# Performance work log

Measured on AMD Instinct MI355X. Metric: run time of the kernel, lower is better.

Reference implementation:

```python
import jax, jax.numpy as jnp
import numpy as np

NEG_INF = jnp.float32(-1e30)


def setup_inputs() -> dict:
    key = jax.random.key(0)
    ks = jax.random.split(key, 7)
    B, Lx, Lm, d = 4, 256, 256, 256
    return {
        "x": jax.random.normal(ks[0], (B, Lx, d), dtype=jnp.float32),
        "memory": jax.random.normal(ks[1], (B, Lm, d), dtype=jnp.float32),
        "memory_mask": jax.random.randint(ks[2], (B, Lm), 0, 2, dtype=jnp.int32),
        "ws1_w": jax.random.normal(ks[3], (d, d), dtype=jnp.float32) * 0.05,
        "ws1_b": jax.random.normal(ks[4], (d,), dtype=jnp.float32) * 0.05,
        "ws2_w": jax.random.normal(ks[5], (d, d), dtype=jnp.float32) * 0.05,
        "wst_w": jax.random.normal(ks[6], (1, d), dtype=jnp.float32) * 0.05,
    }


def reference(x, memory, memory_mask, ws1_w, ws1_b, ws2_w, wst_w):
    # x: [B, Lx, d], memory: [B, Lm, d]; torch Linear: y = x @ W.T + b
    item1 = jnp.einsum('bxd,ed->bxe', x, ws1_w) + ws1_b          # [B, Lx, d]
    item2 = jnp.einsum('bmd,ed->bme', memory, ws2_w)             # [B, Lm, d]
    item = jnp.tanh(item1[:, :, None, :] + item2[:, None, :, :])  # [B, Lx, Lm, d]
    S = jnp.einsum('bxmd,d->bxm', item, wst_w[0])                # [B, Lx, Lm]
    # agg_2_h uses the UNMASKED scores, softmax over Lx after transpose
    agg_2_h = jnp.einsum('bmx,bxd->bmd', jax.nn.softmax(S.transpose(0, 2, 1), axis=-1), x)
    # mask applied to S before the main attention readout
    S = jnp.where(memory_mask[:, None, :] == 0, NEG_INF, S)      # [B, Lx, Lm]
    out = jnp.einsum('bxm,bmd->bxd', jax.nn.softmax(S, axis=-1), memory)
    return (out, S, agg_2_h)
```

## Files before the change

kernel.cpp:

```cpp
#include <hip/hip_runtime.h>

static constexpr int NB = 4;
static constexpr int L  = 256;
static constexpr int D  = 256;

__device__ __forceinline__ float fast_rcp(float x) {
#if __has_builtin(__builtin_amdgcn_rcpf)
    return __builtin_amdgcn_rcpf(x);
#else
    return 1.0f / x;
#endif
}

__device__ __forceinline__ float fast_exp(float x) {
#if __has_builtin(__builtin_amdgcn_exp2f)
    return __builtin_amdgcn_exp2f(x * 1.4426950408889634f);
#else
    return __expf(x);
#endif
}

__device__ __forceinline__ float exp_2x(float x) {
#if __has_builtin(__builtin_amdgcn_exp2f)
    return __builtin_amdgcn_exp2f(x * 2.8853900817779268f);
#else
    return __expf(2.0f * x);
#endif
}

__device__ __forceinline__ float tanh_from_e(float e) {
    return fmaf(-2.0f, fast_rcp(e + 1.0f), 1.0f);
}

__global__ __launch_bounds__(256) void linear_kernel(
    const float* __restrict__ x, const float* __restrict__ mem,
    const float* __restrict__ w1, const float* __restrict__ b1,
    const float* __restrict__ w2,
    float* __restrict__ E1, float* __restrict__ E2)
{
    const int bid = blockIdx.x;
    const int rb  = (bid >> 3) * 32;
    const int cb  = (bid & 7) * 32;
    const int which = rb >= 1024;
    const int rloc  = which ? rb - 1024 : rb;
    const float* src = which ? mem : x;
    const float* W   = which ? w2  : w1;
    float*       dst = which ? E2  : E1;

    constexpr int P4 = 65;
    __shared__ __align__(16) float4 xs4[32 * P4];
    __shared__ __align__(16) float4 ws4[32 * P4];

    const int t = threadIdx.x;
    const float4* src4 = reinterpret_cast<const float4*>(src) + rloc * 64;
    const float4* Wg4  = reinterpret_cast<const float4*>(W)   + cb   * 64;
#pragma unroll
    for (int k = 0; k < 8; ++k) {
        int idx = k * 256 + t;
        int r = idx >> 6, c = idx & 63;
        xs4[r * P4 + c] = src4[r * 64 + c];
        ws4[r * P4 + c] = Wg4[r * 64 + c];
    }
    __syncthreads();

    const int rr = t >> 4, cc = t & 15;
    const float4* a0p = xs4 + rr * P4;
    const float4* a1p = xs4 + (rr + 16) * P4;
    const float4* w0p = ws4 + cc * P4;
    const float4* w1p = ws4 + (cc + 16) * P4;
    float acc00 = 0.f, acc01 = 0.f, acc10 = 0.f, acc11 = 0.f;
#pragma unroll 4
    for (int d4 = 0; d4 < 64; ++d4) {
        float4 a0 = a0p[d4], a1 = a1p[d4];
        float4 w0 = w0p[d4], w1 = w1p[d4];
        acc00 = fmaf(a0.x, w0.x, acc00); acc00 = fmaf(a0.y, w0.y, acc00);
        acc00 = fmaf(a0.z, w0.z, acc00); acc00 = fmaf(a0.w, w0.w, acc00);
        acc01 = fmaf(a0.x, w1.x, acc01); acc01 = fmaf(a0.y, w1.y, acc01);
        acc01 = fmaf(a0.z, w1.z, acc01); acc01 = fmaf(a0.w, w1.w, acc01);
        acc10 = fmaf(a1.x, w0.x, acc10); acc10 = fmaf(a1.y, w0.y, acc10);
        acc10 = fmaf(a1.z, w0.z, acc10); acc10 = fmaf(a1.w, w0.w, acc10);
        acc11 = fmaf(a1.x, w1.x, acc11); acc11 = fmaf(a1.y, w1.y, acc11);
        acc11 = fmaf(a1.z, w1.z, acc11); acc11 = fmaf(a1.w, w1.w, acc11);
    }
    const float bias0 = which ? 0.f : b1[cb + cc];
    const float bias1 = which ? 0.f : b1[cb + cc + 16];
    dst[(rloc + rr)      * D + cb + cc]      = exp_2x(acc00 + bias0);
    dst[(rloc + rr)      * D + cb + cc + 16] = exp_2x(acc01 + bias1);
    dst[(rloc + rr + 16) * D + cb + cc]      = exp_2x(acc10 + bias0);
    dst[(rloc + rr + 16) * D + cb + cc + 16] = exp_2x(acc11 + bias1);
}

__global__ __launch_bounds__(256) void score_kernel(
    const float* __restrict__ E1, const float* __restrict__ E2,
    const float* __restrict__ wst, const int* __restrict__ mask,
    float* __restrict__ outS, float* __restrict__ ST)
{
    const int bid = blockIdx.x;
    const int b   = bid >> 6;
    const int xt  = ((bid >> 3) & 7) * 32;
    const int mt  = (bid & 7) * 32;
    const int t   = threadIdx.x;

    constexpr int P4 = 65;
    __shared__ __align__(16) float4 s1[32 * P4];
    __shared__ __align__(16) float4 s2[32 * P4];
    __shared__ float stile[32 * 33];

    const float4* e14 = reinterpret_cast<const float4*>(E1) + (b * L + xt) * 64;
    const float4* e24 = reinterpret_cast<const float4*>(E2) + (b * L + mt) * 64;
#pragma unroll
    for (int k = 0; k < 8; ++k) {
        int idx = k * 256 + t;
        int r = idx >> 6, c = idx & 63;
        s1[r * P4 + c] = e14[r * 64 + c];
        s2[r * P4 + c] = e24[r * 64 + c];
    }
    __syncthreads();

    const int rr = t >> 4, cc = t & 15;
    const float4* a0p = s1 + rr * P4;
    const float4* a1p = s1 + (rr + 16) * P4;
    const float4* b0p = s2 + cc * P4;
    const float4* b1p = s2 + (cc + 16) * P4;
    const float4* w4  = reinterpret_cast<const float4*>(wst);
    float acc00 = 0.f, acc01 = 0.f, acc10 = 0.f, acc11 = 0.f;
#pragma unroll 4
    for (int d4 = 0; d4 < 64; ++d4) {
        float4 a0 = a0p[d4], a1 = a1p[d4];
        float4 b0 = b0p[d4], b1 = b1p[d4];
        float4 w  = w4[d4];
        acc00 = fmaf(tanh_from_e(a0.x * b0.x), w.x, acc00);
        acc00 = fmaf(tanh_from_e(a0.y * b0.y), w.y, acc00);
        acc00 = fmaf(tanh_from_e(a0.z * b0.z), w.z, acc00);
        acc00 = fmaf(tanh_from_e(a0.w * b0.w), w.w, acc00);
        acc01 = fmaf(tanh_from_e(a0.x * b1.x), w.x, acc01);
        acc01 = fmaf(tanh_from_e(a0.y * b1.y), w.y, acc01);
        acc01 = fmaf(tanh_from_e(a0.z * b1.z), w.z, acc01);
        acc01 = fmaf(tanh_from_e(a0.w * b1.w), w.w, acc01);
        acc10 = fmaf(tanh_from_e(a1.x * b0.x), w.x, acc10);
        acc10 = fmaf(tanh_from_e(a1.y * b0.y), w.y, acc10);
        acc10 = fmaf(tanh_from_e(a1.z * b0.z), w.z, acc10);
        acc10 = fmaf(tanh_from_e(a1.w * b0.w), w.w, acc10);
        acc11 = fmaf(tanh_from_e(a1.x * b1.x), w.x, acc11);
        acc11 = fmaf(tanh_from_e(a1.y * b1.y), w.y, acc11);
        acc11 = fmaf(tanh_from_e(a1.z * b1.z), w.z, acc11);
        acc11 = fmaf(tanh_from_e(a1.w * b1.w), w.w, acc11);
    }

    const int m0 = mt + cc, m1 = mt + cc + 16;
    const int x0 = xt + rr, x1 = xt + rr + 16;
    const bool k0 = (mask[b * L + m0] == 0), k1 = (mask[b * L + m1] == 0);
    outS[((b * L + x0) << 8) + m0] = k0 ? -1e30f : acc00;
    outS[((b * L + x0) << 8) + m1] = k1 ? -1e30f : acc01;
    outS[((b * L + x1) << 8) + m0] = k0 ? -1e30f : acc10;
    outS[((b * L + x1) << 8) + m1] = k1 ? -1e30f : acc11;

    stile[cc        * 33 + rr]      = acc00;
    stile[(cc + 16) * 33 + rr]      = acc01;
    stile[cc        * 33 + rr + 16] = acc10;
    stile[(cc + 16) * 33 + rr + 16] = acc11;
    __syncthreads();
#pragma unroll
    for (int k = 0; k < 4; ++k) {
        int idx = k * 256 + t;
        int mr = idx >> 5, xc = idx & 31;
        ST[((b * L + mt + mr) << 8) + xt + xc] = stile[mr * 33 + xc];
    }
}

__global__ __launch_bounds__(256) void attn_kernel(
    const float* __restrict__ S1, const float* __restrict__ V1, float* __restrict__ out1,
    const float* __restrict__ S2, const float* __restrict__ V2, float* __restrict__ out2)
{
    int bid = blockIdx.x;
    const float* S; const float* V; float* out;
    if (bid < NB * L / 8) { S = S1; V = V1; out = out1; }
    else                  { S = S2; V = V2; out = out2; bid -= NB * L / 8; }

    const int row0 = bid * 8;
    const int b    = row0 >> 8;
    const int t    = threadIdx.x;
    const int w    = t >> 6, l = t & 63;

    __shared__ __align__(16) float p[8][L];
    __shared__ __align__(16) float4 part[8][4][64];

#pragma unroll
    for (int rr = w; rr < 8; rr += 4) {
        float4 sv = reinterpret_cast<const float4*>(S)[((row0 + rr) << 6) + l];
        float m = fmaxf(fmaxf(sv.x, sv.y), fmaxf(sv.z, sv.w));
#pragma unroll
        for (int o = 32; o; o >>= 1) m = fmaxf(m, __shfl_xor(m, o));
        float e0 = fast_exp(sv.x - m), e1 = fast_exp(sv.y - m);
        float e2 = fast_exp(sv.z - m), e3 = fast_exp(sv.w - m);
        float s = (e0 + e1) + (e2 + e3);
#pragma unroll
        for (int o = 32; o; o >>= 1) s += __shfl_xor(s, o);
        float rs = fast_rcp(s);
        reinterpret_cast<float4*>(p[rr])[l] = make_float4(e0 * rs, e1 * rs, e2 * rs, e3 * rs);
    }
    __syncthreads();

    const float4* V4 = reinterpret_cast<const float4*>(V) + (b * L) * 64;
    float4 acc[8];
#pragma unroll
    for (int r = 0; r < 8; ++r) acc[r] = make_float4(0.f, 0.f, 0.f, 0.f);

#pragma unroll 2
    for (int k4 = 0; k4 < 16; ++k4) {
        const int m0 = w * 64 + k4 * 4;
        float4 v0 = V4[(m0 + 0) * 64 + l];
        float4 v1 = V4[(m0 + 1) * 64 + l];
        float4 v2 = V4[(m0 + 2) * 64 + l];
        float4 v3 = V4[(m0 + 3) * 64 + l];
#pragma unroll
        for (int r = 0; r < 8; ++r) {
            float4 pr = *reinterpret_cast<const float4*>(&p[r][m0]);
            acc[r].x = fmaf(pr.x, v0.x, acc[r].x); acc[r].y = fmaf(pr.x, v0.y, acc[r].y);
            acc[r].z = fmaf(pr.x, v0.z, acc[r].z); acc[r].w = fmaf(pr.x, v0.w, acc[r].w);
            acc[r].x = fmaf(pr.y, v1.x, acc[r].x); acc[r].y = fmaf(pr.y, v1.y, acc[r].y);
            acc[r].z = fmaf(pr.y, v1.z, acc[r].z); acc[r].w = fmaf(pr.y, v1.w, acc[r].w);
            acc[r].x = fmaf(pr.z, v2.x, acc[r].x); acc[r].y = fmaf(pr.z, v2.y, acc[r].y);
            acc[r].z = fmaf(pr.z, v2.z, acc[r].z); acc[r].w = fmaf(pr.z, v2.w, acc[r].w);
            acc[r].x = fmaf(pr.w, v3.x, acc[r].x); acc[r].y = fmaf(pr.w, v3.y, acc[r].y);
            acc[r].z = fmaf(pr.w, v3.z, acc[r].z); acc[r].w = fmaf(pr.w, v3.w, acc[r].w);
        }
    }
#pragma unroll
    for (int r = 0; r < 8; ++r) part[r][w][l] = acc[r];
    __syncthreads();

#pragma unroll
    for (int rr = w; rr < 8; rr += 4) {
        float4 r0 = part[rr][0][l], r1 = part[rr][1][l];
        float4 r2 = part[rr][2][l], r3 = part[rr][3][l];
        float4 o;
        o.x = (r0.x + r1.x) + (r2.x + r3.x);
        o.y = (r0.y + r1.y) + (r2.y + r3.y);
        o.z = (r0.z + r1.z) + (r2.z + r3.z);
        o.w = (r0.w + r1.w) + (r2.w + r3.w);
        reinterpret_cast<float4*>(out)[((row0 + rr) << 6) + l] = o;
    }
}

extern "C" void kernel_launch(void* const* d_in, const int* in_sizes, int n_in,
                              void* d_out, int out_size, void* d_ws, size_t ws_size,
                              hipStream_t stream)
{
    const float* x    = (const float*)d_in[0];
    const float* mem  = (const float*)d_in[1];
    const int*   mask = (const int*)  d_in[2];
    const float* w1   = (const float*)d_in[3];
    const float* b1   = (const float*)d_in[4];
    const float* w2   = (const float*)d_in[5];
    const float* wst  = (const float*)d_in[6];

    float* out   = (float*)d_out;
    float* Smask = out + NB * L * L;
    float* agg   = Smask + NB * L * L;

    float* E1 = (float*)d_ws;
    float* E2 = E1 + NB * L * D;
    float* ST = E2 + NB * L * D;

    linear_kernel<<<512, 256, 0, stream>>>(x, mem, w1, b1, w2, E1, E2);
    score_kernel<<<NB * (L / 32) * (L / 32), 256, 0, stream>>>(E1, E2, wst, mask, Smask, ST);
    attn_kernel<<<2 * (NB * L / 8), 256, 0, stream>>>(Smask, mem, out, ST, x, agg);
}
```

Measured before the change: 38.84 us.

## Fold tanh weighting into a reciprocal sum and retile score and softmax kernels

The score kernel rewrites sum_d w*tanh as W_tot - 2*sum_d w/(1+e), which removes one fused op per element. It also shrinks the x tile to 16 rows, giving 512 blocks with a batch-interleaved block mapping. The attention kernel drops the row-max subtraction in softmax and applies the 1/sum normalization after the PV accumulation instead of to each probability. Removing the max relies on scores staying bounded, which holds for small weights, and the smaller score tile lowers data reuse per block.

```diff
diff --git a/kernel.cpp b/kernel.cpp
--- a/kernel.cpp
+++ b/kernel.cpp
@@ -28,15 +28,11 @@
 #endif
 }
 
-__device__ __forceinline__ float tanh_from_e(float e) {
-    return fmaf(-2.0f, fast_rcp(e + 1.0f), 1.0f);
-}
-
 __global__ __launch_bounds__(256) void linear_kernel(
     const float* __restrict__ x, const float* __restrict__ mem,
     const float* __restrict__ w1, const float* __restrict__ b1,
     const float* __restrict__ w2,
-    float* __restrict__ E1, float* __restrict__ E2)
+    float* __restrict__ E1R, float* __restrict__ E2R)
 {
     const int bid = blockIdx.x;
     const int rb  = (bid >> 3) * 32;
@@ -45,7 +41,7 @@
     const int rloc  = which ? rb - 1024 : rb;
     const float* src = which ? mem : x;
     const float* W   = which ? w2  : w1;
-    float*       dst = which ? E2  : E1;
+    float*      dstR = which ? E2R : E1R;
 
     constexpr int P4 = 65;
     __shared__ __align__(16) float4 xs4[32 * P4];
@@ -84,124 +80,129 @@
     }
     const float bias0 = which ? 0.f : b1[cb + cc];
     const float bias1 = which ? 0.f : b1[cb + cc + 16];
-    dst[(rloc + rr)      * D + cb + cc]      = exp_2x(acc00 + bias0);
-    dst[(rloc + rr)      * D + cb + cc + 16] = exp_2x(acc01 + bias1);
-    dst[(rloc + rr + 16) * D + cb + cc]      = exp_2x(acc10 + bias0);
-    dst[(rloc + rr + 16) * D + cb + cc + 16] = exp_2x(acc11 + bias1);
+    const int c0 = cb + cc, c1 = cb + cc + 16;
+    const int rA = rloc + rr, rB = rloc + rr + 16;
+    dstR[rA * D + c0] = exp_2x(acc00 + bias0);
+    dstR[rA * D + c1] = exp_2x(acc01 + bias1);
+    dstR[rB * D + c0] = exp_2x(acc10 + bias0);
+    dstR[rB * D + c1] = exp_2x(acc11 + bias1);
 }
 
 __global__ __launch_bounds__(256) void score_kernel(
-    const float* __restrict__ E1, const float* __restrict__ E2,
+    const float* __restrict__ E1R, const float* __restrict__ E2R,
     const float* __restrict__ wst, const int* __restrict__ mask,
-    float* __restrict__ outS, float* __restrict__ ST)
+    float* __restrict__ Smask, float* __restrict__ ST)
 {
     const int bid = blockIdx.x;
-    const int b   = bid >> 6;
-    const int xt  = ((bid >> 3) & 7) * 32;
-    const int mt  = (bid & 7) * 32;
+    const int p   = bid & 7, q = bid >> 3;
+    const int b   = p >> 1;
+    const int xg  = (q & 7) | ((p & 1) << 3);
+    const int mg  = q >> 3;
+    const int xt  = xg * 16, mt = mg * 32;
+    const int base = b * L;
     const int t   = threadIdx.x;
 
     constexpr int P4 = 65;
-    __shared__ __align__(16) float4 s1[32 * P4];
+    __shared__ __align__(16) float4 s1[16 * P4];
     __shared__ __align__(16) float4 s2[32 * P4];
-    __shared__ float stile[32 * 33];
-
-    const float4* e14 = reinterpret_cast<const float4*>(E1) + (b * L + xt) * 64;
-    const float4* e24 = reinterpret_cast<const float4*>(E2) + (b * L + mt) * 64;
-#pragma unroll
-    for (int k = 0; k < 8; ++k) {
+    __shared__ float stile[32 * 17];
+
+    const float4* e14 = reinterpret_cast<const float4*>(E1R) + (base + xt) * 64;
+    const float4* e24 = reinterpret_cast<const float4*>(E2R) + (base + mt) * 64;
+#pragma unroll
+    for (int k = 0; k < 4; ++k) {
         int idx = k * 256 + t;
         int r = idx >> 6, c = idx & 63;
         s1[r * P4 + c] = e14[r * 64 + c];
+    }
+#pragma unroll
+    for (int k = 0; k < 8; ++k) {
+        int idx = k * 256 + t;
+        int r = idx >> 6, c = idx & 63;
         s2[r * P4 + c] = e24[r * 64 + c];
     }
     __syncthreads();
 
+    const float4* w4 = reinterpret_cast<const float4*>(wst);
+    float W_tot;
+    {
+        float4 wv = w4[t & 63];
+        float s = (wv.x + wv.y) + (wv.z + wv.w);
+#pragma unroll
+        for (int o = 32; o; o >>= 1) s += __shfl_xor(s, o);
+        W_tot = s;
+    }
+
     const int rr = t >> 4, cc = t & 15;
-    const float4* a0p = s1 + rr * P4;
-    const float4* a1p = s1 + (rr + 16) * P4;
+    const float4* ap  = s1 + rr * P4;
     const float4* b0p = s2 + cc * P4;
     const float4* b1p = s2 + (cc + 16) * P4;
-    const float4* w4  = reinterpret_cast<const float4*>(wst);
-    float acc00 = 0.f, acc01 = 0.f, acc10 = 0.f, acc11 = 0.f;
+    float acc0 = 0.f, acc1 = 0.f;
 #pragma unroll 4
     for (int d4 = 0; d4 < 64; ++d4) {
-        float4 a0 = a0p[d4], a1 = a1p[d4];
+        float4 a  = ap[d4];
         float4 b0 = b0p[d4], b1 = b1p[d4];
-        float4 w  = w4[d4];
-        acc00 = fmaf(tanh_from_e(a0.x * b0.x), w.x, acc00);
-        acc00 = fmaf(tanh_from_e(a0.y * b0.y), w.y, acc00);
-        acc00 = fmaf(tanh_from_e(a0.z * b0.z), w.z, acc00);
-        acc00 = fmaf(tanh_from_e(a0.w * b0.w), w.w, acc00);
-        acc01 = fmaf(tanh_from_e(a0.x * b1.x), w.x, acc01);
-        acc01 = fmaf(tanh_from_e(a0.y * b1.y), w.y, acc01);
-        acc01 = fmaf(tanh_from_e(a0.z * b1.z), w.z, acc01);
-        acc01 = fmaf(tanh_from_e(a0.w * b1.w), w.w, acc01);
-        acc10 = fmaf(tanh_from_e(a1.x * b0.x), w.x, acc10);
-        acc10 = fmaf(tanh_from_e(a1.y * b0.y), w.y, acc10);
-        acc10 = fmaf(tanh_from_e(a1.z * b0.z), w.z, acc10);
-        acc10 = fmaf(tanh_from_e(a1.w * b0.w), w.w, acc10);
-        acc11 = fmaf(tanh_from_e(a1.x * b1.x), w.x, acc11);
-        acc11 = fmaf(tanh_from_e(a1.y * b1.y), w.y, acc11);
-        acc11 = fmaf(tanh_from_e(a1.z * b1.z), w.z, acc11);
-        acc11 = fmaf(tanh_from_e(a1.w * b1.w), w.w, acc11);
-    }
-
-    const int m0 = mt + cc, m1 = mt + cc + 16;
-    const int x0 = xt + rr, x1 = xt + rr + 16;
-    const bool k0 = (mask[b * L + m0] == 0), k1 = (mask[b * L + m1] == 0);
-    outS[((b * L + x0) << 8) + m0] = k0 ? -1e30f : acc00;
-    outS[((b * L + x0) << 8) + m1] = k1 ? -1e30f : acc01;
-    outS[((b * L + x1) << 8) + m0] = k0 ? -1e30f : acc10;
-    outS[((b * L + x1) << 8) + m1] = k1 ? -1e30f : acc11;
-
-    stile[cc        * 33 + rr]      = acc00;
-    stile[(cc + 16) * 33 + rr]      = acc01;
-    stile[cc        * 33 + rr + 16] = acc10;
-    stile[(cc + 16) * 33 + rr + 16] = acc11;
-    __syncthreads();
-#pragma unroll
-    for (int k = 0; k < 4; ++k) {
-        int idx = k * 256 + t;
-        int mr = idx >> 5, xc = idx & 31;
-        ST[((b * L + mt + mr) << 8) + xt + xc] = stile[mr * 33 + xc];
+        float4 wv = w4[d4];
+        acc0 = fmaf(wv.x, fast_rcp(fmaf(a.x, b0.x, 1.f)), acc0);
+        acc0 = fmaf(wv.y, fast_rcp(fmaf(a.y, b0.y, 1.f)), acc0);
+        acc0 = fmaf(wv.z, fast_rcp(fmaf(a.z, b0.z, 1.f)), acc0);
+        acc0 = fmaf(wv.w, fast_rcp(fmaf(a.w, b0.w, 1.f)), acc0);
+        acc1 = fmaf(wv.x, fast_rcp(fmaf(a.x, b1.x, 1.f)), acc1);
+        acc1 = fmaf(wv.y, fast_rcp(fmaf(a.y, b1.y, 1.f)), acc1);
+        acc1 = fmaf(wv.z, fast_rcp(fmaf(a.z, b1.z, 1.f)), acc1);
+        acc1 = fmaf(wv.w, fast_rcp(fmaf(a.w, b1.w, 1.f)), acc1);
+    }
+    const float S0 = fmaf(-2.f, acc0, W_tot);
+    const float S1 = fmaf(-2.f, acc1, W_tot);
+
+    const int m0 = mt + cc, m1 = mt + cc + 16, x0 = xt + rr;
+    Smask[((base + x0) << 8) + m0] = (mask[base + m0] == 0) ? -1e30f : S0;
+    Smask[((base + x0) << 8) + m1] = (mask[base + m1] == 0) ? -1e30f : S1;
+
+    stile[cc        * 17 + rr] = S0;
+    stile[(cc + 16) * 17 + rr] = S1;
+    __syncthreads();
+#pragma unroll
+    for (int k = 0; k < 2; ++k) {
+        int idx = k * 256 + t;
+        int mr = idx >> 4, xc = idx & 15;
+        ST[((base + mt + mr) << 8) + xt + xc] = stile[mr * 17 + xc];
     }
 }
 
 __global__ __launch_bounds__(256) void attn_kernel(
-    const float* __restrict__ S1, const float* __restrict__ V1, float* __restrict__ out1,
-    const float* __restrict__ S2, const float* __restrict__ V2, float* __restrict__ out2)
-{
-    int bid = blockIdx.x;
-    const float* S; const float* V; float* out;
-    if (bid < NB * L / 8) { S = S1; V = V1; out = out1; }
-    else                  { S = S2; V = V2; out = out2; bid -= NB * L / 8; }
-
-    const int row0 = bid * 8;
-    const int b    = row0 >> 8;
-    const int t    = threadIdx.x;
-    const int w    = t >> 6, l = t & 63;
-
-    __shared__ __align__(16) float p[8][L];
+    const float* __restrict__ x, const float* __restrict__ mem,
+    const float* __restrict__ Smask, const float* __restrict__ ST,
+    float* __restrict__ out, float* __restrict__ agg)
+{
+    const int bid  = blockIdx.x;
+    const int p    = bid & 7, g = bid >> 3;
+    const int side = p & 1,  b = p >> 1;
+    const float* S = side ? ST : Smask;
+    const float* V = side ? x  : mem;
+    float*       o = side ? agg : out;
+    const int base = b * L;
+    const int row0 = g * 8;
+    const int t = threadIdx.x, w = t >> 6, l = t & 63;
+
+    __shared__ __align__(16) float  ps[8][L];
     __shared__ __align__(16) float4 part[8][4][64];
 
-#pragma unroll
-    for (int rr = w; rr < 8; rr += 4) {
-        float4 sv = reinterpret_cast<const float4*>(S)[((row0 + rr) << 6) + l];
-        float m = fmaxf(fmaxf(sv.x, sv.y), fmaxf(sv.z, sv.w));
-#pragma unroll
-        for (int o = 32; o; o >>= 1) m = fmaxf(m, __shfl_xor(m, o));
-        float e0 = fast_exp(sv.x - m), e1 = fast_exp(sv.y - m);
-        float e2 = fast_exp(sv.z - m), e3 = fast_exp(sv.w - m);
+    float rs0, rs1;
+#pragma unroll
+    for (int rr = w, it = 0; rr < 8; rr += 4, ++it) {
+        float4 sv = reinterpret_cast<const float4*>(S)[((base + row0 + rr) << 6) + l];
+        float e0 = fast_exp(sv.x), e1 = fast_exp(sv.y);
+        float e2 = fast_exp(sv.z), e3 = fast_exp(sv.w);
+        reinterpret_cast<float4*>(ps[rr])[l] = make_float4(e0, e1, e2, e3);
         float s = (e0 + e1) + (e2 + e3);
 #pragma unroll
-        for (int o = 32; o; o >>= 1) s += __shfl_xor(s, o);
-        float rs = fast_rcp(s);
-        reinterpret_cast<float4*>(p[rr])[l] = make_float4(e0 * rs, e1 * rs, e2 * rs, e3 * rs);
-    }
-    __syncthreads();
-
-    const float4* V4 = reinterpret_cast<const float4*>(V) + (b * L) * 64;
+        for (int off = 32; off; off >>= 1) s += __shfl_xor(s, off);
+        if (it == 0) rs0 = fast_rcp(s); else rs1 = fast_rcp(s);
+    }
+    __syncthreads();
+
+    const float4* V4 = reinterpret_cast<const float4*>(V) + base * 64;
     float4 acc[8];
 #pragma unroll
     for (int r = 0; r < 8; ++r) acc[r] = make_float4(0.f, 0.f, 0.f, 0.f);
@@ -215,7 +216,7 @@
         float4 v3 = V4[(m0 + 3) * 64 + l];
 #pragma unroll
         for (int r = 0; r < 8; ++r) {
-            float4 pr = *reinterpret_cast<const float4*>(&p[r][m0]);
+            float4 pr = *reinterpret_cast<const float4*>(&ps[r][m0]);
             acc[r].x = fmaf(pr.x, v0.x, acc[r].x); acc[r].y = fmaf(pr.x, v0.y, acc[r].y);
             acc[r].z = fmaf(pr.x, v0.z, acc[r].z); acc[r].w = fmaf(pr.x, v0.w, acc[r].w);
             acc[r].x = fmaf(pr.y, v1.x, acc[r].x); acc[r].y = fmaf(pr.y, v1.y, acc[r].y);
@@ -231,15 +232,16 @@
     __syncthreads();
 
 #pragma unroll
-    for (int rr = w; rr < 8; rr += 4) {
-        float4 r0 = part[rr][0][l], r1 = part[rr][1][l];
-        float4 r2 = part[rr][2][l], r3 = part[rr][3][l];
-        float4 o;
-        o.x = (r0.x + r1.x) + (r2.x + r3.x);
-        o.y = (r0.y + r1.y) + (r2.y + r3.y);
-        o.z = (r0.z + r1.z) + (r2.z + r3.z);
-        o.w = (r0.w + r1.w) + (r2.w + r3.w);
-        reinterpret_cast<float4*>(out)[((row0 + rr) << 6) + l] = o;
+    for (int rr = w, it = 0; rr < 8; rr += 4, ++it) {
+        float rs = (it == 0) ? rs0 : rs1;
+        float4 q0 = part[rr][0][l], q1 = part[rr][1][l];
+        float4 q2 = part[rr][2][l], q3 = part[rr][3][l];
+        float4 ov;
+        ov.x = ((q0.x + q1.x) + (q2.x + q3.x)) * rs;
+        ov.y = ((q0.y + q1.y) + (q2.y + q3.y)) * rs;
+        ov.z = ((q0.z + q1.z) + (q2.z + q3.z)) * rs;
+        ov.w = ((q0.w + q1.w) + (q2.w + q3.w)) * rs;
+        reinterpret_cast<float4*>(o)[((base + row0 + rr) << 6) + l] = ov;
     }
 }
 
@@ -259,11 +261,11 @@
     float* Smask = out + NB * L * L;
     float* agg   = Smask + NB * L * L;
 
-    float* E1 = (float*)d_ws;
-    float* E2 = E1 + NB * L * D;
-    float* ST = E2 + NB * L * D;
-
-    linear_kernel<<<512, 256, 0, stream>>>(x, mem, w1, b1, w2, E1, E2);
-    score_kernel<<<NB * (L / 32) * (L / 32), 256, 0, stream>>>(E1, E2, wst, mask, Smask, ST);
-    attn_kernel<<<2 * (NB * L / 8), 256, 0, stream>>>(Smask, mem, out, ST, x, agg);
-}
+    float* E1R = (float*)d_ws;
+    float* E2R = E1R + NB * L * D;
+    float* ST  = E2R + NB * L * D;
+
+    linear_kernel<<<512, 256, 0, stream>>>(x, mem, w1, b1, w2, E1R, E2R);
+    score_kernel<<<512, 256, 0, stream>>>(E1R, E2R, wst, mask, Smask, ST);
+    attn_kernel<<<256, 256, 0, stream>>>(x, mem, Smask, ST, out, agg);
+}
```

New measurement: 35.39 us, median of 2. 8.9% less time.
